# Kernel tuning notes

Measured on AMD Instinct MI355X. Metric: run time of the kernel, lower is better.

The kernel has to match this reference:

```python
import jax, jax.numpy as jnp
import numpy as np

S, B, D, H = 1024, 8, 256, 8
DH = D // H
N = S * B
E = 262144
EPS = 1e-5


def setup_inputs():
    key = jax.random.key(0)
    ks = jax.random.split(key, 10)
    g = lambda k, shp, s=0.05: jax.random.normal(k, shp, jnp.float32) * s
    return {
        "x": g(ks[0], (S, B, D), 1.0),
        "condition": g(ks[1], (S, B, 1), 1.0),
        "in_proj_w": g(ks[2], (3 * D, D)),
        "in_proj_b": jnp.zeros((3 * D,), jnp.float32),
        "out_proj_w": g(ks[3], (D, D)),
        "out_proj_b": jnp.zeros((D,), jnp.float32),
        "g1": jnp.ones((D,), jnp.float32), "be1": jnp.zeros((D,), jnp.float32),
        "g2": jnp.ones((D,), jnp.float32), "be2": jnp.zeros((D,), jnp.float32),
        "g3": jnp.ones((D,), jnp.float32), "be3": jnp.zeros((D,), jnp.float32),
        "lin_w": g(ks[4], (D, D)),
        "att_src": g(ks[5], (H, DH)),
        "att_dst": g(ks[6], (H, DH)),
        "gat_bias": jnp.zeros((D,), jnp.float32),
        "w1": g(ks[7], (4 * D, D + 1)),
        "bf1": jnp.zeros((4 * D,), jnp.float32),
        "w2": g(ks[8], (D, 4 * D)),
        "bf2": jnp.zeros((D,), jnp.float32),
        "edge_index": jax.random.randint(ks[9], (2, E), 0, N, jnp.int32),
    }


def _ln(x, g, b):
    m = jnp.mean(x, axis=-1, keepdims=True)
    v = jnp.mean((x - m) ** 2, axis=-1, keepdims=True)
    return (x - m) * jax.lax.rsqrt(v + EPS) * g + b


def _forward(x, condition, in_proj_w, in_proj_b, out_proj_w, out_proj_b,
             g1, be1, g2, be2, g3, be3, lin_w, att_src, att_dst, gat_bias,
             w1, bf1, w2, bf2, edge_index):
    # ---- self-attention (torch MHA, seq-major [S,B,D]) ----
    qkv = jnp.einsum('sbd,ed->sbe', x, in_proj_w) + in_proj_b
    q, k, v = jnp.split(qkv, 3, axis=-1)
    q = q.reshape(S, B, H, DH)
    k = k.reshape(S, B, H, DH)
    v = v.reshape(S, B, H, DH)
    scores = jnp.einsum('sbhd,tbhd->bhst', q, k) / np.float32(np.sqrt(DH))
    a = jax.nn.softmax(scores, axis=-1)
    ctx = jnp.einsum('bhst,tbhd->sbhd', a, v).reshape(S, B, D)
    attn_out = ctx @ out_proj_w.T + out_proj_b
    x1 = _ln(x + attn_out, g1, be1)
    # ---- GATConv over flattened (batch-major) nodes ----
    xr = x1.transpose(1, 0, 2).reshape(N, D)          # node i = b*S + s
    xh = (xr @ lin_w.T).reshape(N, H, DH)
    loops = jnp.arange(N, dtype=edge_index.dtype)     # PyG add_self_loops=True
    src = jnp.concatenate([edge_index[0], loops])
    dst = jnp.concatenate([edge_index[1], loops])
    a_src = jnp.sum(xh * att_src, axis=-1)            # [N,H]
    a_dst = jnp.sum(xh * att_dst, axis=-1)
    e = jax.nn.leaky_relu(a_src[src] + a_dst[dst], 0.2)  # [Et,H]
    m = jax.ops.segment_max(e, dst, num_segments=N)
    ee = jnp.exp(e - m[dst])
    z = jax.ops.segment_sum(ee, dst, num_segments=N)
    alpha = ee / z[dst]
    msg = xh[src] * alpha[:, :, None]                 # [Et,H,DH]
    gout = jax.ops.segment_sum(msg, dst, num_segments=N).reshape(N, D) + gat_bias
    gout = gout.reshape(B, S, D).transpose(1, 0, 2)
    x2 = _ln(x1 + gout, g2, be2)
    # ---- conditioned FFN ----
    xc = jnp.concatenate([x2, condition], axis=-1)    # [S,B,D+1]
    h = jax.nn.relu(xc @ w1.T + bf1)
    f = h @ w2.T + bf2
    return _ln(x2 + f, g3, be3)


def reference(x, condition, in_proj_w, in_proj_b, out_proj_w, out_proj_b,
              g1, be1, g2, be2, g3, be3, lin_w, att_src, att_dst, gat_bias,
              w1, bf1, w2, bf2, edge_index):
    return _forward(x, condition, in_proj_w, in_proj_b, out_proj_w, out_proj_b,
                    g1, be1, g2, be2, g3, be3, lin_w, att_src, att_dst, gat_bias,
                    w1, bf1, w2, bf2, edge_index)
```

## Files before the change

### kernel.cpp

```cpp
#include <hip/hip_runtime.h>
#include <hip/hip_bf16.h>

#define S_ 1024
#define B_ 8
#define D_ 256
#define H_ 8
#define DH_ 32
#define N_ 8192
#define E_ 262144
#define ET_ 270336

typedef unsigned short u16;
typedef float f32x4 __attribute__((ext_vector_type(4)));
typedef __bf16 bf16x8 __attribute__((ext_vector_type(8)));
typedef short s16x4 __attribute__((ext_vector_type(4)));

#define QK_SCALE 0.17677669529663687f

__device__ inline u16 f2bf(float v) {
    unsigned int u = __float_as_uint(v);
    u = (u + 0x7fffu + ((u >> 16) & 1u)) >> 16;
    return (u16)u;
}
__device__ inline float bf2f(u16 u) { return __uint_as_float(((unsigned int)u) << 16); }

__device__ inline unsigned int pack_trunc(float lo, float hi) {
    return __builtin_amdgcn_perm(__float_as_uint(hi), __float_as_uint(lo), 0x07060302u);
}

__device__ inline void gload16(const u16* g, u16* l) {
    __builtin_amdgcn_global_load_lds((const __attribute__((address_space(1))) unsigned int*)g,
                                     (__attribute__((address_space(3))) unsigned int*)l, 16, 0, 0);
}

__device__ inline f32x4 mfma16bf(s16x4 a, s16x4 b, f32x4 c) {
#if __has_builtin(__builtin_amdgcn_mfma_f32_16x16x16bf16_1k)
    return __builtin_amdgcn_mfma_f32_16x16x16bf16_1k(a, b, c, 0, 0, 0);
#else
    asm volatile("v_mfma_f32_16x16x16_bf16 %0, %1, %2, %0" : "+v"(c) : "v"(a), "v"(b));
    return c;
#endif
}

__global__ __launch_bounds__(256) void convert_all(const float* __restrict__ x,  const float* __restrict__ wi,
                                                   const float* __restrict__ wo, const float* __restrict__ wl,
                                                   const float* __restrict__ w1, const float* __restrict__ w2,
                                                   u16* __restrict__ Xbf, u16* __restrict__ Wi, u16* __restrict__ Wo,
                                                   u16* __restrict__ Wl, u16* __restrict__ W1, u16* __restrict__ W2,
                                                   int* __restrict__ count, int* __restrict__ cursor)
{
    const int idx = blockIdx.x * 256 + threadIdx.x;
    const int C0 = 2097152;
    const int C1 = C0 + 196608;
    const int C2 = C1 + 65536;
    const int C3 = C2 + 65536;
    const int C4 = C3 + 294912;
    const int C5 = C4 + 262144;
    const int C6 = C5 + 16384;
    if (idx < C0)      { Xbf[idx] = f2bf(x[idx]); }
    else if (idx < C1) { int i = idx - C0; Wi[i] = f2bf(wi[i]); }
    else if (idx < C2) { int i = idx - C1; Wo[i] = f2bf(wo[i]); }
    else if (idx < C3) { int i = idx - C2; Wl[i] = f2bf(wl[i]); }
    else if (idx < C4) { int i = idx - C3; int r = i / 288, k = i - r * 288;
                         W1[i] = (k < 257) ? f2bf(w1[r * 257 + k]) : (u16)0; }
    else if (idx < C5) { int i = idx - C4; W2[i] = f2bf(w2[i]); }
    else if (idx < C6) { int i = idx - C5; if (i < 8192) count[i] = 0; else cursor[i - 8192] = 0; }
}

__global__ __launch_bounds__(256) void gemm_qkv_hist(const u16* __restrict__ A,
                                                     const u16* __restrict__ W,
                                                     const float* __restrict__ bias,
                                                     u16* __restrict__ Cv,
                                                     const int* __restrict__ ei, int* __restrict__ count)
{
    const int tid = threadIdx.x;
    if (blockIdx.x >= 768) {
        const int e = (blockIdx.x - 768) * 256 + tid;
        const int dst = (e < E_) ? ei[E_ + e] : e - E_;
        atomicAdd(&count[dst], 1);
        return;
    }
    __shared__ u16 As[2][128 * 32];
    __shared__ u16 Bs[2][64 * 32];
    const int m0 = (blockIdx.x / 12) * 128, n0 = (blockIdx.x % 12) * 64;
    const int lane = tid & 63, w = tid >> 6;
    const int wm = w >> 1, wn = w & 1;
    const int lr = lane & 15, lg = lane >> 4;

    f32x4 acc[4][2] = {};

    const u16* Ag = A + (size_t)(m0 + (tid >> 2)) * 256 + (tid & 3) * 8;
    const u16* Wg = W + (size_t)(n0 + (tid >> 2)) * 256 + (tid & 3) * 8;

    auto stage = [&](int buf, int k0) {
        gload16(Ag + k0,                    &As[buf][tid * 8]);
        gload16(Ag + (size_t)64 * 256 + k0, &As[buf][64 * 32 + tid * 8]);
        gload16(Wg + k0,                    &Bs[buf][tid * 8]);
    };
    stage(0, 0);
    __syncthreads();
    int cur = 0;
    for (int kt = 0; kt < 8; ++kt) {
        if (kt + 1 < 8) stage(cur ^ 1, (kt + 1) << 5);
        bf16x8 af[4], bg[2];
        #pragma unroll
        for (int i = 0; i < 4; ++i) af[i] = *(const bf16x8*)&As[cur][(wm * 64 + i * 16 + lr) * 32 + lg * 8];
        #pragma unroll
        for (int i = 0; i < 2; ++i) bg[i] = *(const bf16x8*)&Bs[cur][(wn * 32 + i * 16 + lr) * 32 + lg * 8];
        #pragma unroll
        for (int mi = 0; mi < 4; ++mi)
            #pragma unroll
            for (int ni = 0; ni < 2; ++ni)
                acc[mi][ni] = __builtin_amdgcn_mfma_f32_16x16x32_bf16(af[mi], bg[ni], acc[mi][ni], 0, 0, 0);
        __syncthreads();
        cur ^= 1;
    }
    #pragma unroll
    for (int mi = 0; mi < 4; ++mi)
        #pragma unroll
        for (int ni = 0; ni < 2; ++ni) {
            const int col = n0 + wn * 32 + ni * 16 + lr;
            const float bv = bias[col];
            const int part = col >> 8, hh = (col >> 5) & 7, dh = col & 31;
            #pragma unroll
            for (int r = 0; r < 4; ++r) {
                const int row = m0 + wm * 64 + mi * 16 + lg * 4 + r;
                const int ss = row >> 3, bb = row & 7;
                Cv[(((size_t)((part * 8 + bb) * 8 + hh)) * 1024 + ss) * 32 + dh] = f2bf(acc[mi][ni][r] + bv);
            }
        }
}

__global__ __launch_bounds__(512) void attn_mfma(const u16* __restrict__ qkv, u16* __restrict__ ctx,
                                                 const int* __restrict__ count, int* __restrict__ offset)
{
    const int tid = threadIdx.x;
    if (blockIdx.x == 512) {
        __shared__ int s[512];
        const int base = tid * 16;
        int c[16]; int sum = 0;
        #pragma unroll
        for (int i = 0; i < 16; ++i) { c[i] = count[base + i]; sum += c[i]; }
        s[tid] = sum; __syncthreads();
        for (int off = 1; off < 512; off <<= 1) {
            int add = (tid >= off) ? s[tid - off] : 0;
            __syncthreads();
            s[tid] += add;
            __syncthreads();
        }
        int run = (tid == 0) ? 0 : s[tid - 1];
        #pragma unroll
        for (int i = 0; i < 16; ++i) { offset[base + i] = run; run += c[i]; }
        if (tid == 511) offset[8192] = run;
        return;
    }
    const int qt = blockIdx.x & 7, bh = blockIdx.x >> 3;
    const int b = bh >> 3, h = bh & 7;
    const int lane = tid & 63, w = tid >> 6;
    const int c = lane & 15, g = lane >> 4;

    __shared__ __align__(16) u16 Ks[2][128][40];
    __shared__ __align__(16) u16 Vt[2][32][132];

    const size_t plane = (size_t)(b * 8 + h) * 32768;
    const int q0 = qt * 128 + w * 16;
    const bf16x8 qf = *(const bf16x8*)&qkv[plane + (size_t)(q0 + c) * 32 + g * 8];
    const u16* kbase = qkv + 2097152 + plane;

    auto stage = [&](int buf, int kt) {
        const int r = tid >> 2, c0 = (tid & 3) * 8;
        const u16* kp = kbase + (size_t)(kt * 128 + r) * 32 + c0;
        *(uint4*)&Ks[buf][r][c0] = *(const uint4*)kp;
        u16 vb[8];
        *(uint4*)vb = *(const uint4*)(kp + 2097152);
        #pragma unroll
        for (int i = 0; i < 8; ++i) Vt[buf][c0 + i][r] = vb[i];
    };

    float l = 0.f;
    f32x4 o0 = {}, o1 = {};

    stage(0, 0);
    __syncthreads();
    int cur = 0;
    for (int kt = 0; kt < 8; ++kt) {
        if (kt + 1 < 8) stage(cur ^ 1, kt + 1);
        f32x4 sc[8];
        #pragma unroll
        for (int t = 0; t < 8; ++t) {
            const bf16x8 kf = *(const bf16x8*)&Ks[cur][t * 16 + c][g * 8];
            sc[t] = __builtin_amdgcn_mfma_f32_16x16x32_bf16(kf, qf, (f32x4){0.f, 0.f, 0.f, 0.f}, 0, 0, 0);
        }
        unsigned int pb[8][2];
        float ls = 0.f;
        #pragma unroll
        for (int t = 0; t < 8; ++t) {
            const float p0 = __expf(sc[t][0] * QK_SCALE);
            const float p1 = __expf(sc[t][1] * QK_SCALE);
            const float p2 = __expf(sc[t][2] * QK_SCALE);
            const float p3 = __expf(sc[t][3] * QK_SCALE);
            ls += (p0 + p1) + (p2 + p3);
            pb[t][0] = pack_trunc(p0, p1);
            pb[t][1] = pack_trunc(p2, p3);
        }
        l += ls;
        #pragma unroll
        for (int t = 0; t < 8; ++t) {
            union { unsigned int u[2]; s16x4 v; } pu;
            pu.u[0] = pb[t][0]; pu.u[1] = pb[t][1];
            const s16x4 vf0 = *(const s16x4*)&Vt[cur][c][t * 16 + g * 4];
            const s16x4 vf1 = *(const s16x4*)&Vt[cur][16 + c][t * 16 + g * 4];
            o0 = mfma16bf(vf0, pu.v, o0);
            o1 = mfma16bf(vf1, pu.v, o1);
        }
        __syncthreads();
        cur ^= 1;
    }
    l += __shfl_xor(l, 16, 64);
    l += __shfl_xor(l, 32, 64);
    const float inv = 1.f / l;
    u16 ob[8];
    #pragma unroll
    for (int r = 0; r < 4; ++r) { ob[r] = f2bf(o0[r] * inv); ob[4 + r] = f2bf(o1[r] * inv); }
    const size_t obase = ((size_t)(q0 + c) * 8 + b) * 256 + h * 32 + g * 4;
    *(uint2*)&ctx[obase]      = *(uint2*)ob;
    *(uint2*)&ctx[obase + 16] = *(uint2*)(ob + 4);
}

template<int MODE>
__global__ __launch_bounds__(512) void gemm_ln(const u16* __restrict__ A, int lda,
                                               const u16* __restrict__ W, int ldw, int Ksz,
                                               const float* __restrict__ bias,
                                               const float* __restrict__ resid,
                                               const float* __restrict__ gamma,
                                               const float* __restrict__ beta,
                                               const float* __restrict__ att_s,
                                               const float* __restrict__ att_d,
                                               float* __restrict__ outf,
                                               u16* __restrict__ outn,
                                               float* __restrict__ asrc,
                                               float* __restrict__ adst,
                                               const int* __restrict__ ei,
                                               const int* __restrict__ offset,
                                               int* __restrict__ cursor,
                                               int* __restrict__ sorted)
{
    constexpr int BM = 32;
    const int tid = threadIdx.x;
    if (MODE == 0 && blockIdx.x >= 256) {
        const int e = (blockIdx.x - 256) * 512 + tid;
        int src, dst;
        if (e < E_) { src = ei[e]; dst = ei[E_ + e]; }
        else        { src = dst = e - E_; }
        const int pos = offset[dst] + atomicAdd(&cursor[dst], 1);
        sorted[pos] = src;
        return;
    }
    __shared__ u16 As[2][BM * 32];
    __shared__ u16 Bs[2][256 * 32];
    __shared__ float2 red[BM][8];
    const int m0 = blockIdx.x * BM;
    const int lane = tid & 63, w = tid >> 6;
    const int rw = w >> 2, cw = w & 3;
    const int lr = lane & 15, lg = lane >> 4;

    f32x4 acc[4] = {};

    auto stage = [&](int buf, int k0) {
        #pragma unroll
        for (int j = 0; j < 2; ++j) {
            const int idx = tid + j * 512;
            gload16(W + (size_t)(idx >> 2) * ldw + (idx & 3) * 8 + k0, &Bs[buf][idx * 8]);
        }
        if (tid < BM * 4)
            gload16(A + (size_t)(m0 + (tid >> 2)) * lda + (tid & 3) * 8 + k0, &As[buf][tid * 8]);
    };
    stage(0, 0);
    __syncthreads();
    const int nt = Ksz >> 5;
    int cur = 0;
    for (int kt = 0; kt < nt; ++kt) {
        if (kt + 1 < nt) stage(cur ^ 1, (kt + 1) << 5);
        bf16x8 af = *(const bf16x8*)&As[cur][(rw * 16 + lr) * 32 + lg * 8];
        bf16x8 bg[4];
        #pragma unroll
        for (int i = 0; i < 4; ++i)  bg[i] = *(const bf16x8*)&Bs[cur][(cw * 64 + i * 16 + lr) * 32 + lg * 8];
        #pragma unroll
        for (int ni = 0; ni < 4; ++ni)
            acc[ni] = __builtin_amdgcn_mfma_f32_16x16x32_bf16(af, bg[ni], acc[ni], 0, 0, 0);
        __syncthreads();
        cur ^= 1;
    }
    int col[4]; float gam[4], bet[4], bv[4], asv[4], adv[4];
    #pragma unroll
    for (int ni = 0; ni < 4; ++ni) {
        col[ni] = cw * 64 + ni * 16 + lr;
        if (MODE != 1) { gam[ni] = gamma[col[ni]]; bet[ni] = beta[col[ni]]; bv[ni] = bias[col[ni]]; }
        else           { asv[ni] = att_s[col[ni]]; adv[ni] = att_d[col[ni]]; }
    }
    #pragma unroll
    for (int r = 0; r < 4; ++r) {
        const int row = rw * 16 + lg * 4 + r;
        const int grow = m0 + row;
        float s1 = 0.f, s2 = 0.f;
        float2 sp0 = {0.f, 0.f}, sp1 = {0.f, 0.f};
        #pragma unroll
        for (int ni = 0; ni < 4; ++ni) {
            float v = acc[ni][r];
            if (MODE != 1) v += bv[ni] + resid[(size_t)grow * 256 + col[ni]];
            acc[ni][r] = v;
            if (MODE == 1) {
                if (ni < 2) { sp0.x += v * asv[ni]; sp0.y += v * adv[ni]; }
                else        { sp1.x += v * asv[ni]; sp1.y += v * adv[ni]; }
            } else { s1 += v; s2 += v * v; }
        }
        #pragma unroll
        for (int msk = 1; msk < 16; msk <<= 1) {
            if (MODE == 1) {
                sp0.x += __shfl_xor(sp0.x, msk, 64); sp0.y += __shfl_xor(sp0.y, msk, 64);
                sp1.x += __shfl_xor(sp1.x, msk, 64); sp1.y += __shfl_xor(sp1.y, msk, 64);
            } else { s1 += __shfl_xor(s1, msk, 64); s2 += __shfl_xor(s2, msk, 64); }
        }
        if (lr == 0) {
            if (MODE == 1) { red[row][cw * 2] = sp0; red[row][cw * 2 + 1] = sp1; }
            else           { red[row][cw] = (float2){s1, s2}; }
        }
    }
    __syncthreads();
    if (MODE == 1) {
        #pragma unroll
        for (int r = 0; r < 4; ++r) {
            const int grow = m0 + rw * 16 + lg * 4 + r;
            #pragma unroll
            for (int ni = 0; ni < 4; ++ni)
                outn[(size_t)grow * 256 + col[ni]] = f2bf(acc[ni][r]);
        }
        for (int idx = tid; idx < BM * 8; idx += 512) {
            const int row = idx >> 3, h = idx & 7;
            asrc[(size_t)(m0 + row) * 8 + h] = red[row][h].x;
            adst[(size_t)(m0 + row) * 8 + h] = red[row][h].y;
        }
    } else {
        #pragma unroll
        for (int r = 0; r < 4; ++r) {
            const int row = rw * 16 + lg * 4 + r;
            const int grow = m0 + row;
            const float2 t0 = red[row][0], t1 = red[row][1], t2 = red[row][2], t3 = red[row][3];
            const float mean = (t0.x + t1.x + t2.x + t3.x) * (1.f / 256.f);
            const float var  = (t0.y + t1.y + t2.y + t3.y) * (1.f / 256.f) - mean * mean;
            const float rs = rsqrtf(var + 1e-5f);
            #pragma unroll
            for (int ni = 0; ni < 4; ++ni) {
                const float o = (acc[ni][r] - mean) * rs * gam[ni] + bet[ni];
                outf[(size_t)grow * 256 + col[ni]] = o;
                if (MODE == 0) {
                    const int node = (grow & 7) * 1024 + (grow >> 3);
                    outn[(size_t)node * 256 + col[ni]] = f2bf(o);
                }
            }
        }
    }
}

__global__ __launch_bounds__(256) void gat_gather_ln(const int* __restrict__ sorted, const int* __restrict__ offset,
                                                     const float* __restrict__ asrc, const float* __restrict__ adst,
                                                     const u16* __restrict__ xh,
                                                     const float* __restrict__ X1f, const float* __restrict__ gb,
                                                     const float* __restrict__ g2, const float* __restrict__ be2,
                                                     const float* __restrict__ cond,
                                                     float* __restrict__ X2f, u16* __restrict__ X2pad)
{
    const int wid = threadIdx.x >> 6, lane = threadIdx.x & 63;
    const int pair = wid >> 1, half = wid & 1;
    const int dst = blockIdx.x * 2 + pair;
    const int sub = lane >> 5, l32 = lane & 31;
    const int h = l32 >> 2;
    const float ad = adst[dst * 8 + h];
    const int beg = offset[dst], end = offset[dst + 1];
    const int mid = beg + ((end - beg + 1) >> 1);
    const int b0 = half ? mid : beg;
    const int b1 = half ? end : mid;

    __shared__ float szs[2][8];
    __shared__ __align__(16) float sa[2][32][8];

    float z = 0.f;
    float a[8] = {};
    #pragma unroll 2
    for (int i = b0 + sub; i < b1; i += 2) {
        const int src = sorted[i];
        float e = asrc[src * 8 + h] + ad;
        e = fmaxf(e, 0.2f * e);
        const float p = __expf(e);
        z += p;
        const uint4 xv = *(const uint4*)&xh[(size_t)src * 256 + l32 * 8];
        a[0] += p * __uint_as_float(xv.x << 16);
        a[1] += p * __uint_as_float(xv.x & 0xffff0000u);
        a[2] += p * __uint_as_float(xv.y << 16);
        a[3] += p * __uint_as_float(xv.y & 0xffff0000u);
        a[4] += p * __uint_as_float(xv.z << 16);
        a[5] += p * __uint_as_float(xv.z & 0xffff0000u);
        a[6] += p * __uint_as_float(xv.w << 16);
        a[7] += p * __uint_as_float(xv.w & 0xffff0000u);
    }
    z += __shfl_xor(z, 32, 64);
    #pragma unroll
    for (int j = 0; j < 8; ++j) a[j] += __shfl_xor(a[j], 32, 64);
    if (half && sub == 0) {
        if ((l32 & 3) == 0) szs[pair][h] = z;
        *(f32x4*)&sa[pair][l32][0] = (f32x4){a[0], a[1], a[2], a[3]};
        *(f32x4*)&sa[pair][l32][4] = (f32x4){a[4], a[5], a[6], a[7]};
    }
    __syncthreads();
    if (half) return;
    const float zt = z + szs[pair][h];
    const float inv = 1.f / zt;
    const int row = (dst & 1023) * 8 + (dst >> 10);
    float v[8];
    {
        const f32x4 x0 = *(const f32x4*)&X1f[(size_t)row * 256 + l32 * 8];
        const f32x4 x1 = *(const f32x4*)&X1f[(size_t)row * 256 + l32 * 8 + 4];
        const f32x4 gb0 = *(const f32x4*)&gb[l32 * 8];
        const f32x4 gb1 = *(const f32x4*)&gb[l32 * 8 + 4];
        const f32x4 m0 = *(const f32x4*)&sa[pair][l32][0];
        const f32x4 m1 = *(const f32x4*)&sa[pair][l32][4];
        #pragma unroll
        for (int j = 0; j < 4; ++j) {
            v[j]     = x0[j] + (a[j] + m0[j]) * inv + gb0[j];
            v[4 + j] = x1[j] + (a[4 + j] + m1[j]) * inv + gb1[j];
        }
    }
    float s1 = 0.f, s2 = 0.f;
    #pragma unroll
    for (int j = 0; j < 8; ++j) { s1 += v[j]; s2 += v[j] * v[j]; }
    #pragma unroll
    for (int msk = 1; msk < 32; msk <<= 1) { s1 += __shfl_xor(s1, msk, 64); s2 += __shfl_xor(s2, msk, 64); }
    const float mean = s1 * (1.f / 256.f);
    const float var = s2 * (1.f / 256.f) - mean * mean;
    const float rs = rsqrtf(var + 1e-5f);
    if (sub == 0) {
        const f32x4 gg0 = *(const f32x4*)&g2[l32 * 8];
        const f32x4 gg1 = *(const f32x4*)&g2[l32 * 8 + 4];
        const f32x4 be0 = *(const f32x4*)&be2[l32 * 8];
        const f32x4 be1 = *(const f32x4*)&be2[l32 * 8 + 4];
        f32x4 o0, o1;
        u16 ob[8];
        #pragma unroll
        for (int j = 0; j < 4; ++j) {
            o0[j] = (v[j] - mean) * rs * gg0[j] + be0[j];
            o1[j] = (v[4 + j] - mean) * rs * gg1[j] + be1[j];
            ob[j] = f2bf(o0[j]); ob[4 + j] = f2bf(o1[j]);
        }
        *(f32x4*)&X2f[(size_t)row * 256 + l32 * 8]     = o0;
        *(f32x4*)&X2f[(size_t)row * 256 + l32 * 8 + 4] = o1;
        *(uint4*)&X2pad[(size_t)row * 288 + l32 * 8] = *(uint4*)ob;
        if (l32 < 8) {
            u16 zz[4] = {0, 0, 0, 0};
            if (l32 == 0) zz[0] = f2bf(cond[row]);
            *(uint2*)&X2pad[(size_t)row * 288 + 256 + l32 * 4] = *(uint2*)zz;
        }
    }
}

__global__ __launch_bounds__(256) void gemm_w1(const u16* __restrict__ A,
                                               const u16* __restrict__ W,
                                               const float* __restrict__ bias,
                                               u16* __restrict__ Cv)
{
    __shared__ u16 As[2][128 * 32];
    __shared__ u16 Bs[2][128 * 32];
    const int tid = threadIdx.x;
    const int m0 = blockIdx.y * 128, n0 = blockIdx.x * 128;
    const int lane = tid & 63, w = tid >> 6;
    const int wm = w >> 1, wn = w & 1;
    const int lr = lane & 15, lg = lane >> 4;

    f32x4 acc[4][4] = {};

    const u16* Ag = A + (size_t)(m0 + (tid >> 2)) * 288 + (tid & 3) * 8;
    const u16* Wg = W + (size_t)(n0 + (tid >> 2)) * 288 + (tid & 3) * 8;

    auto stage = [&](int buf, int k0) {
        gload16(Ag + k0,                    &As[buf][tid * 8]);
        gload16(Ag + (size_t)64 * 288 + k0, &As[buf][64 * 32 + tid * 8]);
        gload16(Wg + k0,                    &Bs[buf][tid * 8]);
        gload16(Wg + (size_t)64 * 288 + k0, &Bs[buf][64 * 32 + tid * 8]);
    };
    stage(0, 0);
    __syncthreads();
    int cur = 0;
    for (int kt = 0; kt < 9; ++kt) {
        if (kt + 1 < 9) stage(cur ^ 1, (kt + 1) << 5);
        bf16x8 af[4], bg[4];
        #pragma unroll
        for (int i = 0; i < 4; ++i) {
            af[i] = *(const bf16x8*)&As[cur][(wm * 64 + i * 16 + lr) * 32 + lg * 8];
            bg[i] = *(const bf16x8*)&Bs[cur][(wn * 64 + i * 16 + lr) * 32 + lg * 8];
        }
        #pragma unroll
        for (int mi = 0; mi < 4; ++mi)
            #pragma unroll
            for (int ni = 0; ni < 4; ++ni)
                acc[mi][ni] = __builtin_amdgcn_mfma_f32_16x16x32_bf16(af[mi], bg[ni], acc[mi][ni], 0, 0, 0);
        __syncthreads();
        cur ^= 1;
    }
    #pragma unroll
    for (int mi = 0; mi < 4; ++mi)
        #pragma unroll
        for (int ni = 0; ni < 4; ++ni) {
            const int col = n0 + wn * 64 + ni * 16 + lr;
            const float bv = bias[col];
            #pragma unroll
            for (int r = 0; r < 4; ++r) {
                const int row = m0 + wm * 64 + mi * 16 + lg * 4 + r;
                Cv[(size_t)row * 1024 + col] = f2bf(fmaxf(acc[mi][ni][r] + bv, 0.f));
            }
        }
}

extern "C" void kernel_launch(void* const* d_in, const int* in_sizes, int n_in,
                              void* d_out, int out_size, void* d_ws, size_t ws_size,
                              hipStream_t stream)
{
    const float* x          = (const float*)d_in[0];
    const float* condition  = (const float*)d_in[1];
    const float* in_proj_w  = (const float*)d_in[2];
    const float* in_proj_b  = (const float*)d_in[3];
    const float* out_proj_w = (const float*)d_in[4];
    const float* out_proj_b = (const float*)d_in[5];
    const float* g1         = (const float*)d_in[6];
    const float* be1        = (const float*)d_in[7];
    const float* g2         = (const float*)d_in[8];
    const float* be2        = (const float*)d_in[9];
    const float* g3         = (const float*)d_in[10];
    const float* be3        = (const float*)d_in[11];
    const float* lin_w      = (const float*)d_in[12];
    const float* att_src    = (const float*)d_in[13];
    const float* att_dst    = (const float*)d_in[14];
    const float* gat_bias   = (const float*)d_in[15];
    const float* w1         = (const float*)d_in[16];
    const float* bf1        = (const float*)d_in[17];
    const float* w2         = (const float*)d_in[18];
    const float* bf2        = (const float*)d_in[19];
    const int*   edge_index = (const int*)d_in[20];
    float* out = (float*)d_out;

    char* ws = (char*)d_ws;
    u16*   QKV    = (u16*)(ws + 0);
    u16*   Hb     = (u16*)(ws + 0);
    u16*   CTX    = (u16*)(ws + 16777216);
    u16*   X1node = (u16*)(ws + 20971520);
    u16*   XH     = (u16*)(ws + 25165824);
    float* X1f    = (float*)(ws + 29360128);
    float* X2f    = (float*)(ws + 37748736);
    u16*   X2pad  = (u16*)(ws + 46137344);
    u16*   Xbf    = (u16*)(ws + 50855936);
    float* ASRC   = (float*)(ws + 55050240);
    float* ADST   = (float*)(ws + 55312384);
    u16*   W_inp  = (u16*)(ws + 55574528);
    u16*   W_out  = (u16*)(ws + 55967744);
    u16*   W_lin  = (u16*)(ws + 56098816);
    u16*   W_w1   = (u16*)(ws + 56229888);
    u16*   W_w2   = (u16*)(ws + 56819712);
    int*   COUNT  = (int*)(ws + 57344000);
    int*   OFFSET = (int*)(ws + 57376768);
    int*   CURSOR = (int*)(ws + 57413632);
    int*   SORTED = (int*)(ws + 57446400);

    convert_all<<<11712, 256, 0, stream>>>(x, in_proj_w, out_proj_w, lin_w, w1, w2,
                                           Xbf, W_inp, W_out, W_lin, W_w1, W_w2, COUNT, CURSOR);
    gemm_qkv_hist<<<1824, 256, 0, stream>>>(Xbf, W_inp, in_proj_b, QKV, edge_index, COUNT);
    attn_mfma<<<513, 512, 0, stream>>>(QKV, CTX, COUNT, OFFSET);
    gemm_ln<0><<<784, 512, 0, stream>>>(CTX, 256, W_out, 256, 256, out_proj_b, x, g1, be1,
                                        nullptr, nullptr, X1f, X1node, nullptr, nullptr,
                                        edge_index, OFFSET, CURSOR, SORTED);
    gemm_ln<1><<<256, 512, 0, stream>>>(X1node, 256, W_lin, 256, 256, nullptr, nullptr, nullptr, nullptr,
                                        att_src, att_dst, nullptr, XH, ASRC, ADST,
                                        nullptr, nullptr, nullptr, nullptr);
    gat_gather_ln<<<4096, 256, 0, stream>>>(SORTED, OFFSET, ASRC, ADST, XH,
                                            X1f, gat_bias, g2, be2, condition, X2f, X2pad);
    gemm_w1<<<dim3(8, 64), 256, 0, stream>>>(X2pad, W_w1, bf1, Hb);
    gemm_ln<2><<<256, 512, 0, stream>>>(Hb, 1024, W_w2, 1024, 1024, bf2, X2f, g3, be3,
                                        nullptr, nullptr, out, nullptr, nullptr, nullptr,
                                        nullptr, nullptr, nullptr, nullptr);
}
```

Before: 138.7 us.

## Halve GEMM-LN row tile and spread GAT gather over eight warp groups per node

```diff
diff --git a/kernel.cpp b/kernel.cpp
--- a/kernel.cpp
+++ b/kernel.cpp
@@ -245,10 +245,10 @@
                                                int* __restrict__ cursor,
                                                int* __restrict__ sorted)
 {
-    constexpr int BM = 32;
+    constexpr int BM = 16;
     const int tid = threadIdx.x;
-    if (MODE == 0 && blockIdx.x >= 256) {
-        const int e = (blockIdx.x - 256) * 512 + tid;
+    if (MODE == 0 && blockIdx.x >= 512) {
+        const int e = (blockIdx.x - 512) * 512 + tid;
         int src, dst;
         if (e < E_) { src = ei[e]; dst = ei[E_ + e]; }
         else        { src = dst = e - E_; }
@@ -261,10 +261,9 @@
     __shared__ float2 red[BM][8];
     const int m0 = blockIdx.x * BM;
     const int lane = tid & 63, w = tid >> 6;
-    const int rw = w >> 2, cw = w & 3;
     const int lr = lane & 15, lg = lane >> 4;
 
-    f32x4 acc[4] = {};
+    f32x4 acc[2] = {};
 
     auto stage = [&](int buf, int k0) {
         #pragma unroll
@@ -281,58 +280,55 @@
     int cur = 0;
     for (int kt = 0; kt < nt; ++kt) {
         if (kt + 1 < nt) stage(cur ^ 1, (kt + 1) << 5);
-        bf16x8 af = *(const bf16x8*)&As[cur][(rw * 16 + lr) * 32 + lg * 8];
-        bf16x8 bg[4];
-        #pragma unroll
-        for (int i = 0; i < 4; ++i)  bg[i] = *(const bf16x8*)&Bs[cur][(cw * 64 + i * 16 + lr) * 32 + lg * 8];
-        #pragma unroll
-        for (int ni = 0; ni < 4; ++ni)
+        const bf16x8 af = *(const bf16x8*)&As[cur][lr * 32 + lg * 8];
+        bf16x8 bg[2];
+        #pragma unroll
+        for (int i = 0; i < 2; ++i)
+            bg[i] = *(const bf16x8*)&Bs[cur][(w * 32 + i * 16 + lr) * 32 + lg * 8];
+        #pragma unroll
+        for (int ni = 0; ni < 2; ++ni)
             acc[ni] = __builtin_amdgcn_mfma_f32_16x16x32_bf16(af, bg[ni], acc[ni], 0, 0, 0);
         __syncthreads();
         cur ^= 1;
     }
-    int col[4]; float gam[4], bet[4], bv[4], asv[4], adv[4];
-    #pragma unroll
-    for (int ni = 0; ni < 4; ++ni) {
-        col[ni] = cw * 64 + ni * 16 + lr;
+    int col[2]; float gam[2], bet[2], bv[2], asv[2], adv[2];
+    #pragma unroll
+    for (int ni = 0; ni < 2; ++ni) {
+        col[ni] = w * 32 + ni * 16 + lr;
         if (MODE != 1) { gam[ni] = gamma[col[ni]]; bet[ni] = beta[col[ni]]; bv[ni] = bias[col[ni]]; }
         else           { asv[ni] = att_s[col[ni]]; adv[ni] = att_d[col[ni]]; }
     }
     #pragma unroll
     for (int r = 0; r < 4; ++r) {
-        const int row = rw * 16 + lg * 4 + r;
+        const int row = lg * 4 + r;
         const int grow = m0 + row;
         float s1 = 0.f, s2 = 0.f;
-        float2 sp0 = {0.f, 0.f}, sp1 = {0.f, 0.f};
-        #pragma unroll
-        for (int ni = 0; ni < 4; ++ni) {
+        float2 sp = {0.f, 0.f};
+        #pragma unroll
+        for (int ni = 0; ni < 2; ++ni) {
             float v = acc[ni][r];
             if (MODE != 1) v += bv[ni] + resid[(size_t)grow * 256 + col[ni]];
             acc[ni][r] = v;
-            if (MODE == 1) {
-                if (ni < 2) { sp0.x += v * asv[ni]; sp0.y += v * adv[ni]; }
-                else        { sp1.x += v * asv[ni]; sp1.y += v * adv[ni]; }
-            } else { s1 += v; s2 += v * v; }
+            if (MODE == 1) { sp.x += v * asv[ni]; sp.y += v * adv[ni]; }
+            else           { s1 += v; s2 += v * v; }
         }
         #pragma unroll
         for (int msk = 1; msk < 16; msk <<= 1) {
-            if (MODE == 1) {
-                sp0.x += __shfl_xor(sp0.x, msk, 64); sp0.y += __shfl_xor(sp0.y, msk, 64);
-                sp1.x += __shfl_xor(sp1.x, msk, 64); sp1.y += __shfl_xor(sp1.y, msk, 64);
-            } else { s1 += __shfl_xor(s1, msk, 64); s2 += __shfl_xor(s2, msk, 64); }
+            if (MODE == 1) { sp.x += __shfl_xor(sp.x, msk, 64); sp.y += __shfl_xor(sp.y, msk, 64); }
+            else           { s1 += __shfl_xor(s1, msk, 64); s2 += __shfl_xor(s2, msk, 64); }
         }
         if (lr == 0) {
-            if (MODE == 1) { red[row][cw * 2] = sp0; red[row][cw * 2 + 1] = sp1; }
-            else           { red[row][cw] = (float2){s1, s2}; }
+            if (MODE == 1) red[row][w] = sp;
+            else           red[row][w] = (float2){s1, s2};
         }
     }
     __syncthreads();
     if (MODE == 1) {
         #pragma unroll
         for (int r = 0; r < 4; ++r) {
-            const int grow = m0 + rw * 16 + lg * 4 + r;
-            #pragma unroll
-            for (int ni = 0; ni < 4; ++ni)
+            const int grow = m0 + lg * 4 + r;
+            #pragma unroll
+            for (int ni = 0; ni < 2; ++ni)
                 outn[(size_t)grow * 256 + col[ni]] = f2bf(acc[ni][r]);
         }
         for (int idx = tid; idx < BM * 8; idx += 512) {
@@ -343,14 +339,16 @@
     } else {
         #pragma unroll
         for (int r = 0; r < 4; ++r) {
-            const int row = rw * 16 + lg * 4 + r;
+            const int row = lg * 4 + r;
             const int grow = m0 + row;
-            const float2 t0 = red[row][0], t1 = red[row][1], t2 = red[row][2], t3 = red[row][3];
-            const float mean = (t0.x + t1.x + t2.x + t3.x) * (1.f / 256.f);
-            const float var  = (t0.y + t1.y + t2.y + t3.y) * (1.f / 256.f) - mean * mean;
+            float ts1 = 0.f, ts2 = 0.f;
+            #pragma unroll
+            for (int j = 0; j < 8; ++j) { ts1 += red[row][j].x; ts2 += red[row][j].y; }
+            const float mean = ts1 * (1.f / 256.f);
+            const float var  = ts2 * (1.f / 256.f) - mean * mean;
             const float rs = rsqrtf(var + 1e-5f);
             #pragma unroll
-            for (int ni = 0; ni < 4; ++ni) {
+            for (int ni = 0; ni < 2; ++ni) {
                 const float o = (acc[ni][r] - mean) * rs * gam[ni] + bet[ni];
                 outf[(size_t)grow * 256 + col[ni]] = o;
                 if (MODE == 0) {
@@ -370,24 +368,19 @@
                                                      const float* __restrict__ cond,
                                                      float* __restrict__ X2f, u16* __restrict__ X2pad)
 {
-    const int wid = threadIdx.x >> 6, lane = threadIdx.x & 63;
-    const int pair = wid >> 1, half = wid & 1;
-    const int dst = blockIdx.x * 2 + pair;
-    const int sub = lane >> 5, l32 = lane & 31;
+    const int tid = threadIdx.x;
+    const int dst = blockIdx.x;
+    const int grp = tid >> 5, l32 = tid & 31;
     const int h = l32 >> 2;
     const float ad = adst[dst * 8 + h];
     const int beg = offset[dst], end = offset[dst + 1];
-    const int mid = beg + ((end - beg + 1) >> 1);
-    const int b0 = half ? mid : beg;
-    const int b1 = half ? end : mid;
-
-    __shared__ float szs[2][8];
-    __shared__ __align__(16) float sa[2][32][8];
+
+    __shared__ float szs[8][8];
+    __shared__ __align__(16) float sa[8][32][8];
 
     float z = 0.f;
     float a[8] = {};
-    #pragma unroll 2
-    for (int i = b0 + sub; i < b1; i += 2) {
+    for (int i = beg + grp; i < end; i += 8) {
         const int src = sorted[i];
         float e = asrc[src * 8 + h] + ad;
         e = fmaxf(e, 0.2f * e);
@@ -403,17 +396,21 @@
         a[6] += p * __uint_as_float(xv.w << 16);
         a[7] += p * __uint_as_float(xv.w & 0xffff0000u);
     }
-    z += __shfl_xor(z, 32, 64);
-    #pragma unroll
-    for (int j = 0; j < 8; ++j) a[j] += __shfl_xor(a[j], 32, 64);
-    if (half && sub == 0) {
-        if ((l32 & 3) == 0) szs[pair][h] = z;
-        *(f32x4*)&sa[pair][l32][0] = (f32x4){a[0], a[1], a[2], a[3]};
-        *(f32x4*)&sa[pair][l32][4] = (f32x4){a[4], a[5], a[6], a[7]};
-    }
+    if ((l32 & 3) == 0) szs[grp][h] = z;
+    *(f32x4*)&sa[grp][l32][0] = (f32x4){a[0], a[1], a[2], a[3]};
+    *(f32x4*)&sa[grp][l32][4] = (f32x4){a[4], a[5], a[6], a[7]};
     __syncthreads();
-    if (half) return;
-    const float zt = z + szs[pair][h];
+    if (tid >= 32) return;
+    float zt = 0.f;
+    float at[8] = {};
+    #pragma unroll
+    for (int g = 0; g < 8; ++g) {
+        zt += szs[g][h];
+        const f32x4 m0 = *(const f32x4*)&sa[g][l32][0];
+        const f32x4 m1 = *(const f32x4*)&sa[g][l32][4];
+        #pragma unroll
+        for (int j = 0; j < 4; ++j) { at[j] += m0[j]; at[4 + j] += m1[j]; }
+    }
     const float inv = 1.f / zt;
     const int row = (dst & 1023) * 8 + (dst >> 10);
     float v[8];
@@ -422,12 +419,10 @@
         const f32x4 x1 = *(const f32x4*)&X1f[(size_t)row * 256 + l32 * 8 + 4];
         const f32x4 gb0 = *(const f32x4*)&gb[l32 * 8];
         const f32x4 gb1 = *(const f32x4*)&gb[l32 * 8 + 4];
-        const f32x4 m0 = *(const f32x4*)&sa[pair][l32][0];
-        const f32x4 m1 = *(const f32x4*)&sa[pair][l32][4];
         #pragma unroll
         for (int j = 0; j < 4; ++j) {
-            v[j]     = x0[j] + (a[j] + m0[j]) * inv + gb0[j];
-            v[4 + j] = x1[j] + (a[4 + j] + m1[j]) * inv + gb1[j];
+            v[j]     = x0[j] + at[j] * inv + gb0[j];
+            v[4 + j] = x1[j] + at[4 + j] * inv + gb1[j];
         }
     }
     float s1 = 0.f, s2 = 0.f;
@@ -438,27 +433,25 @@
     const float mean = s1 * (1.f / 256.f);
     const float var = s2 * (1.f / 256.f) - mean * mean;
     const float rs = rsqrtf(var + 1e-5f);
-    if (sub == 0) {
-        const f32x4 gg0 = *(const f32x4*)&g2[l32 * 8];
-        const f32x4 gg1 = *(const f32x4*)&g2[l32 * 8 + 4];
-        const f32x4 be0 = *(const f32x4*)&be2[l32 * 8];
-        const f32x4 be1 = *(const f32x4*)&be2[l32 * 8 + 4];
-        f32x4 o0, o1;
-        u16 ob[8];
-        #pragma unroll
-        for (int j = 0; j < 4; ++j) {
-            o0[j] = (v[j] - mean) * rs * gg0[j] + be0[j];
-            o1[j] = (v[4 + j] - mean) * rs * gg1[j] + be1[j];
-            ob[j] = f2bf(o0[j]); ob[4 + j] = f2bf(o1[j]);
-        }
-        *(f32x4*)&X2f[(size_t)row * 256 + l32 * 8]     = o0;
-        *(f32x4*)&X2f[(size_t)row * 256 + l32 * 8 + 4] = o1;
-        *(uint4*)&X2pad[(size_t)row * 288 + l32 * 8] = *(uint4*)ob;
-        if (l32 < 8) {
-            u16 zz[4] = {0, 0, 0, 0};
-            if (l32 == 0) zz[0] = f2bf(cond[row]);
-            *(uint2*)&X2pad[(size_t)row * 288 + 256 + l32 * 4] = *(uint2*)zz;
-        }
+    const f32x4 gg0 = *(const f32x4*)&g2[l32 * 8];
+    const f32x4 gg1 = *(const f32x4*)&g2[l32 * 8 + 4];
+    const f32x4 be0 = *(const f32x4*)&be2[l32 * 8];
+    const f32x4 be1 = *(const f32x4*)&be2[l32 * 8 + 4];
+    f32x4 o0, o1;
+    u16 ob[8];
+    #pragma unroll
+    for (int j = 0; j < 4; ++j) {
+        o0[j] = (v[j] - mean) * rs * gg0[j] + be0[j];
+        o1[j] = (v[4 + j] - mean) * rs * gg1[j] + be1[j];
+        ob[j] = f2bf(o0[j]); ob[4 + j] = f2bf(o1[j]);
+    }
+    *(f32x4*)&X2f[(size_t)row * 256 + l32 * 8]     = o0;
+    *(f32x4*)&X2f[(size_t)row * 256 + l32 * 8 + 4] = o1;
+    *(uint4*)&X2pad[(size_t)row * 288 + l32 * 8] = *(uint4*)ob;
+    if (l32 < 8) {
+        u16 zz[4] = {0, 0, 0, 0};
+        if (l32 == 0) zz[0] = f2bf(cond[row]);
+        *(uint2*)&X2pad[(size_t)row * 288 + 256 + l32 * 4] = *(uint2*)zz;
     }
 }
 
@@ -572,16 +565,16 @@
                                            Xbf, W_inp, W_out, W_lin, W_w1, W_w2, COUNT, CURSOR);
     gemm_qkv_hist<<<1824, 256, 0, stream>>>(Xbf, W_inp, in_proj_b, QKV, edge_index, COUNT);
     attn_mfma<<<513, 512, 0, stream>>>(QKV, CTX, COUNT, OFFSET);
-    gemm_ln<0><<<784, 512, 0, stream>>>(CTX, 256, W_out, 256, 256, out_proj_b, x, g1, be1,
-                                        nullptr, nullptr, X1f, X1node, nullptr, nullptr,
-                                        edge_index, OFFSET, CURSOR, SORTED);
-    gemm_ln<1><<<256, 512, 0, stream>>>(X1node, 256, W_lin, 256, 256, nullptr, nullptr, nullptr, nullptr,
+    gemm_ln<0><<<1040, 512, 0, stream>>>(CTX, 256, W_out, 256, 256, out_proj_b, x, g1, be1,
+                                         nullptr, nullptr, X1f, X1node, nullptr, nullptr,
+                                         edge_index, OFFSET, CURSOR, SORTED);
+    gemm_ln<1><<<512, 512, 0, stream>>>(X1node, 256, W_lin, 256, 256, nullptr, nullptr, nullptr, nullptr,
                                         att_src, att_dst, nullptr, XH, ASRC, ADST,
                                         nullptr, nullptr, nullptr, nullptr);
-    gat_gather_ln<<<4096, 256, 0, stream>>>(SORTED, OFFSET, ASRC, ADST, XH,
+    gat_gather_ln<<<8192, 256, 0, stream>>>(SORTED, OFFSET, ASRC, ADST, XH,
                                             X1f, gat_bias, g2, be2, condition, X2f, X2pad);
     gemm_w1<<<dim3(8, 64), 256, 0, stream>>>(X2pad, W_w1, bf1, Hb);
-    gemm_ln<2><<<256, 512, 0, stream>>>(Hb, 1024, W_w2, 1024, 1024, bf2, X2f, g3, be3,
+    gemm_ln<2><<<512, 512, 0, stream>>>(Hb, 1024, W_w2, 1024, 1024, bf2, X2f, g3, be3,
                                         nullptr, nullptr, out, nullptr, nullptr, nullptr,
                                         nullptr, nullptr, nullptr, nullptr);
 }
```

After: 141.4 us. No clear change (+1.9%).
